# Kernel optimization log

Hardware: AMD Instinct MI355X
Metric: run time of the kernel (lower is better)

## Reference

```python
import jax, jax.numpy as jnp
import numpy as np


def silu(x):
    return x * jax.nn.sigmoid(x)


def setup_inputs() -> dict:
    key = jax.random.key(0)
    ks = jax.random.split(key, 12)
    B, S, Dm = 2, 2048, 768
    I, N, R, K = 1536, 16, 48, 4
    s = 0.02
    return {
        "input_states": jax.random.normal(ks[0], (B, S, Dm), jnp.float32),
        "in_proj_w": jax.random.normal(ks[1], (2 * I, Dm), jnp.float32) * s,
        "conv_w": jax.random.normal(ks[2], (I, 1, K), jnp.float32) * s,
        "conv_b": jax.random.normal(ks[3], (I,), jnp.float32) * s,
        "x_proj_w": jax.random.normal(ks[4], (R + 2 * N, I), jnp.float32) * s,
        "dt_proj_w": jax.random.normal(ks[5], (I, R), jnp.float32) * s,
        "dt_proj_b": jax.random.normal(ks[6], (I,), jnp.float32) * s,
        "A_log": jax.random.normal(ks[7], (I, N), jnp.float32) * 0.5,
        "D": jax.random.normal(ks[8], (I,), jnp.float32) * s,
        "out_proj_w": jax.random.normal(ks[9], (Dm, I), jnp.float32) * s,
        "alpha": jax.random.uniform(ks[10], (I,), jnp.float32),
        "feature_gating": jax.random.uniform(ks[11], (I,), jnp.float32),
    }


def reference(input_states, in_proj_w, conv_w, conv_b, x_proj_w,
              dt_proj_w, dt_proj_b, A_log, D, out_proj_w,
              alpha, feature_gating):
    Bsz, S, _ = input_states.shape
    I, N = A_log.shape
    R = dt_proj_w.shape[1]
    K = conv_w.shape[-1]

    # in_proj (no bias), chunk into hidden / gate, each [B, I, S]
    proj = jnp.einsum('bsd,ed->bse', input_states, in_proj_w)  # [B, S, 2I]
    hidden, gate = jnp.split(proj.transpose(0, 2, 1), 2, axis=1)

    # causal depthwise conv1d + SiLU
    h = jax.lax.conv_general_dilated(
        hidden, conv_w, window_strides=(1,), padding=[(K - 1, 0)],
        dimension_numbers=('NCH', 'OIH', 'NCH'), feature_group_count=I)
    h = silu(h + conv_b[None, :, None])  # [B, I, S]

    # x_proj -> time_step, B, C
    ssm_p = jnp.einsum('bis,ei->bse', h, x_proj_w)  # [B, S, R+2N]
    ts, Bm, Cm = jnp.split(ssm_p, [R, R + N], axis=-1)

    dt = jax.nn.softplus(jnp.einsum('bsr,ir->bsi', ts, dt_proj_w) + dt_proj_b)
    dt = dt.transpose(0, 2, 1)                       # [B, I, S]
    dt = dt.at[:, :, -1].multiply(alpha[None, :])    # alpha scales last step

    A = -jnp.exp(A_log.astype(jnp.float32))          # [I, N]
    dA = jnp.exp(A[None, :, None, :] * dt[:, :, :, None])       # [B, I, S, N]
    dBu = dt[:, :, :, None] * Bm[:, None, :, :] * h[:, :, :, None]  # [B, I, S, N]

    def step(state, xs):
        dA_t, dBu_t, C_t = xs
        state = dA_t * state + dBu_t                 # [B, I, N]
        y = jnp.einsum('bin,bn->bi', state, C_t)
        return state, y

    init = jnp.zeros((Bsz, I, N), input_states.dtype)
    _, ys = jax.lax.scan(
        step, init,
        (dA.transpose(2, 0, 1, 3), dBu.transpose(2, 0, 1, 3), Cm.transpose(1, 0, 2)))
    y = ys.transpose(1, 2, 0)                        # [B, I, S]

    y = (y + h * D[None, :, None]) * silu(gate)
    y = y.at[:, :, -1].multiply(feature_gating[None, :])
    return jnp.einsum('bis,di->bsd', y, out_proj_w)  # [B, S, Dm]
```

## Files before the change

kernel.cpp:

```cpp
#include <hip/hip_runtime.h>
#include <math.h>


static constexpr int S_LEN  = 2048;
static constexpr int DMODEL = 768;
static constexpr int ICH    = 1536;
static constexpr int NST    = 16;
static constexpr int MROWS  = 4096;
static constexpr int NCH    = 64;
static constexpr int CHS    = 32;
static constexpr int CSTR   = 2 * ICH * NST;

typedef _Float16 f16;
typedef f16 f16x8 __attribute__((ext_vector_type(8)));
typedef f16 f16x4 __attribute__((ext_vector_type(4)));
typedef f16 f16x2 __attribute__((ext_vector_type(2)));
typedef float f32x4 __attribute__((ext_vector_type(4)));

#if __has_builtin(__builtin_amdgcn_exp2f)
#define EXP2F(x) __builtin_amdgcn_exp2f(x)
#else
#define EXP2F(x) exp2f(x)
#endif

typedef __attribute__((address_space(3))) void lds_void;
typedef const __attribute__((address_space(1))) void glb_void;

__device__ __forceinline__ void glds16(f16* l, const f16* g) {
    __builtin_amdgcn_global_load_lds((glb_void*)g, (lds_void*)l, 16, 0, 0);
}

__device__ __forceinline__ float silu_f(float x) {
    return x / (1.0f + __expf(-x));
}

__global__ __launch_bounds__(256) void prep(
    const float* __restrict__ s0, f16* __restrict__ d0, int n0,
    const float* __restrict__ s1, f16* __restrict__ d1, int n1,
    float* __restrict__ z)
{
    int i = (blockIdx.x * 256 + threadIdx.x) * 4;
    if (i < n0) {
        float4 v = *(const float4*)(s0 + i);
        f16x4 o = { (f16)v.x, (f16)v.y, (f16)v.z, (f16)v.w };
        *(f16x4*)(d0 + i) = o;
    } else if (i < n0 + n1) {
        int j = i - n0;
        float4 v = *(const float4*)(s1 + j);
        f16x4 o = { (f16)v.x, (f16)v.y, (f16)v.z, (f16)v.w };
        *(f16x4*)(d1 + j) = o;
    } else {
        int j = i - n0 - n1;
        float4 zv = {};
        *(float4*)(z + j) = zv;
    }
}

__global__ __launch_bounds__(256) void k1m(
    const f16* __restrict__ Xh,
    const f16* __restrict__ Wh,
    f16* __restrict__ hidden,
    f16* __restrict__ sgate)
{
    __shared__ __align__(16) f16 As[2][128 * 32];
    __shared__ __align__(16) f16 Bs[2][64 * 32];
    const int tid = threadIdx.x;
    const int lane = tid & 63, wave = tid >> 6;
    const int quad = lane >> 4, l16 = lane & 15;
    const int wm = wave & 1, wn = wave >> 1;
    const int m0 = blockIdx.x * 128, n0 = blockIdx.y * 64;
    const int l_row = lane >> 2, l_c8 = (lane & 3) * 8;

    const f16* Ag = Xh + (size_t)(m0 + wave * 16 + l_row) * 768 + l_c8;
    const f16* Bg = Wh + (size_t)(n0 + wave * 16 + l_row) * 768 + l_c8;
    const int aLo = (wave * 16) * 32, aHi = (64 + wave * 16) * 32;
    const int bOff = (wave * 16) * 32;

#define K1_STAGE(buf, kk)                                        \
    do {                                                         \
        glds16(&As[buf][aLo], Ag + (kk));                        \
        glds16(&As[buf][aHi], Ag + (size_t)64 * 768 + (kk));     \
        glds16(&Bs[buf][bOff], Bg + (kk));                       \
    } while (0)

#define K1_COMPUTE(buf)                                                        \
    do {                                                                       \
        f16x8 af[4], bf[2];                                                    \
        _Pragma("unroll")                                                      \
        for (int mi = 0; mi < 4; ++mi)                                         \
            af[mi] = *(const f16x8*)&As[buf][(wm * 64 + mi * 16 + l16) * 32 + quad * 8]; \
        _Pragma("unroll")                                                      \
        for (int ni = 0; ni < 2; ++ni)                                         \
            bf[ni] = *(const f16x8*)&Bs[buf][(wn * 32 + ni * 16 + l16) * 32 + quad * 8]; \
        _Pragma("unroll")                                                      \
        for (int mi = 0; mi < 4; ++mi)                                         \
            _Pragma("unroll")                                                  \
            for (int ni = 0; ni < 2; ++ni)                                     \
                acc[mi][ni] = __builtin_amdgcn_mfma_f32_16x16x32_f16(          \
                    af[mi], bf[ni], acc[mi][ni], 0, 0, 0);                     \
    } while (0)

    K1_STAGE(0, 0);
    __syncthreads();

    f32x4 acc[4][2] = {};
    for (int k0 = 0; k0 < 768; k0 += 64) {
        K1_STAGE(1, k0 + 32);
        K1_COMPUTE(0);
        __syncthreads();
        if (k0 + 64 < 768) K1_STAGE(0, k0 + 64);
        K1_COMPUTE(1);
        __syncthreads();
    }
#undef K1_STAGE
#undef K1_COMPUTE

    const bool isGate = (n0 >= ICH);
    f16* outp = isGate ? sgate : hidden;
    const int e0 = (isGate ? (n0 - ICH) : n0) + wn * 32 + l16;
    #pragma unroll
    for (int mi = 0; mi < 4; ++mi) {
        #pragma unroll
        for (int ni = 0; ni < 2; ++ni) {
            #pragma unroll
            for (int r = 0; r < 4; ++r) {
                int m = m0 + wm * 64 + mi * 16 + quad * 4 + r;
                int e = e0 + ni * 16;
                float v = acc[mi][ni][r];
                if (isGate) v = silu_f(v);
                outp[(size_t)m * ICH + e] = (f16)v;
            }
        }
    }
}

__global__ __launch_bounds__(256) void k3m(
    const f16* __restrict__ hidden,
    const float* __restrict__ conv_w,
    const float* __restrict__ conv_b,
    const float* __restrict__ xw,
    f16* __restrict__ h,
    float* __restrict__ ssmp)
{
    __shared__ __align__(16) f16 Ah[128 * 32];
    __shared__ __align__(16) f16 Bh[80 * 32];
    __shared__ float4 cwv[96];
    __shared__ float  cbv[96];
    const int tid = threadIdx.x;
    const int lane = tid & 63, wave = tid >> 6;
    const int quad = lane >> 4, l16 = lane & 15;
    const int m0 = blockIdx.x * 128;
    const int kbeg = blockIdx.y * 96;

    if (tid < 96) {
        cwv[tid] = *(const float4*)(conv_w + (size_t)(kbeg + tid) * 4);
        cbv[tid] = conv_b[kbeg + tid];
    }

    f32x4 acc[2][5] = {};
    for (int k0 = kbeg; k0 < kbeg + 96; k0 += 32) {
        __syncthreads();
        #pragma unroll
        for (int it = 0; it < 2; ++it) {
            int slot = tid + it * 256;
            int r_ = slot >> 2, c_ = (slot & 3) * 8;
            int gm = m0 + r_, c = k0 + c_;
            int s = gm & (S_LEN - 1);
            const f16* bp = hidden + (size_t)gm * ICH + c;
            f16x8 x0 = *(const f16x8*)bp;
            f16x8 x1 = *(const f16x8*)(bp - (s >= 1 ? ICH : 0));
            f16x8 x2 = *(const f16x8*)(bp - (s >= 2 ? 2 * ICH : 0));
            f16x8 x3 = *(const f16x8*)(bp - (s >= 3 ? 3 * ICH : 0));
            f16x8 o;
            #pragma unroll
            for (int j = 0; j < 8; ++j) {
                int ci = (k0 - kbeg) + c_ + j;
                float4 w = cwv[ci];
                float v1 = (s >= 1) ? (float)x1[j] : 0.f;
                float v2 = (s >= 2) ? (float)x2[j] : 0.f;
                float v3 = (s >= 3) ? (float)x3[j] : 0.f;
                float r = cbv[ci] + w.x * v3 + w.y * v2 + w.z * v1 + w.w * (float)x0[j];
                o[j] = (f16)silu_f(r);
            }
            *(f16x8*)&Ah[r_ * 32 + c_] = o;
            *(f16x8*)(h + (size_t)gm * ICH + c) = o;
        }
        {
            int c4 = (tid & 7) * 4;
            for (int r = tid >> 3; r < 80; r += 32) {
                float4 v = *(const float4*)(xw + (size_t)r * ICH + k0 + c4);
                f16x4 o = { (f16)v.x, (f16)v.y, (f16)v.z, (f16)v.w };
                *(f16x4*)&Bh[r * 32 + c4] = o;
            }
        }
        __syncthreads();
        f16x8 af[2], bf[5];
        #pragma unroll
        for (int mi = 0; mi < 2; ++mi)
            af[mi] = *(const f16x8*)&Ah[(wave * 32 + mi * 16 + l16) * 32 + quad * 8];
        #pragma unroll
        for (int j = 0; j < 5; ++j)
            bf[j] = *(const f16x8*)&Bh[(j * 16 + l16) * 32 + quad * 8];
        #pragma unroll
        for (int mi = 0; mi < 2; ++mi)
            #pragma unroll
            for (int j = 0; j < 5; ++j)
                acc[mi][j] = __builtin_amdgcn_mfma_f32_16x16x32_f16(
                    af[mi], bf[j], acc[mi][j], 0, 0, 0);
    }
    #pragma unroll
    for (int mi = 0; mi < 2; ++mi) {
        #pragma unroll
        for (int j = 0; j < 5; ++j) {
            #pragma unroll
            for (int r = 0; r < 4; ++r) {
                int m = m0 + wave * 32 + mi * 16 + quad * 4 + r;
                atomicAdd(ssmp + (size_t)m * 80 + j * 16 + l16, acc[mi][j][r]);
            }
        }
    }
}

__global__ __launch_bounds__(256) void k4m(
    const float* __restrict__ ssmp,
    const float* __restrict__ dtw,
    const float* __restrict__ dtb,
    const float* __restrict__ alpha,
    f16* __restrict__ dt)
{
    __shared__ __align__(16) f16 As[128 * 72];
    __shared__ __align__(16) f16 Bs[128 * 72];
    const int tid = threadIdx.x;
    const int lane = tid & 63, wave = tid >> 6;
    const int quad = lane >> 4, l16 = lane & 15;
    const int wm = wave & 1, wn = wave >> 1;
    const int m0 = blockIdx.x * 128, n0 = blockIdx.y * 128;
    const int srow = tid >> 1;
    const int shalf = tid & 1;

    {
        const float* sa = ssmp + (size_t)(m0 + srow) * 80 + shalf * 24;
        const float* sb = dtw + (size_t)(n0 + srow) * 48 + shalf * 24;
        f16* da = &As[srow * 72 + shalf * 24];
        f16* db = &Bs[srow * 72 + shalf * 24];
        #pragma unroll
        for (int j = 0; j < 6; ++j) {
            float4 va = *(const float4*)(sa + 4 * j);
            float4 vb = *(const float4*)(sb + 4 * j);
            f16x4 oa = { (f16)va.x, (f16)va.y, (f16)va.z, (f16)va.w };
            f16x4 ob = { (f16)vb.x, (f16)vb.y, (f16)vb.z, (f16)vb.w };
            *(f16x4*)(da + 4 * j) = oa;
            *(f16x4*)(db + 4 * j) = ob;
        }
        if (shalf) {
            f16x8 z = {};
            *(f16x8*)&As[srow * 72 + 48] = z;
            *(f16x8*)&As[srow * 72 + 56] = z;
            *(f16x8*)&Bs[srow * 72 + 48] = z;
            *(f16x8*)&Bs[srow * 72 + 56] = z;
        }
    }
    __syncthreads();

    f32x4 acc[4][4] = {};
    #pragma unroll
    for (int ks = 0; ks < 2; ++ks) {
        f16x8 af[4], bf[4];
        #pragma unroll
        for (int mi = 0; mi < 4; ++mi)
            af[mi] = *(const f16x8*)&As[(wm * 64 + mi * 16 + l16) * 72 + ks * 32 + quad * 8];
        #pragma unroll
        for (int ni = 0; ni < 4; ++ni)
            bf[ni] = *(const f16x8*)&Bs[(wn * 64 + ni * 16 + l16) * 72 + ks * 32 + quad * 8];
        #pragma unroll
        for (int mi = 0; mi < 4; ++mi)
            #pragma unroll
            for (int ni = 0; ni < 4; ++ni)
                acc[mi][ni] = __builtin_amdgcn_mfma_f32_16x16x32_f16(
                    af[mi], bf[ni], acc[mi][ni], 0, 0, 0);
    }

    #pragma unroll
    for (int ni = 0; ni < 4; ++ni) {
        int e = n0 + wn * 64 + ni * 16 + l16;
        float bias = dtb[e];
        float al = alpha[e];
        #pragma unroll
        for (int mi = 0; mi < 4; ++mi) {
            #pragma unroll
            for (int r = 0; r < 4; ++r) {
                int m = m0 + wm * 64 + mi * 16 + quad * 4 + r;
                float x = acc[mi][ni][r] + bias;
                float sp = (x > 20.0f) ? x : __logf(1.0f + __expf(x));
                if ((m & (S_LEN - 1)) == S_LEN - 1) sp *= al;
                dt[(size_t)m * ICH + e] = (f16)sp;
            }
        }
    }
}

__global__ __launch_bounds__(256) void k5a_chunk(
    const f16* __restrict__ dt,
    const f16* __restrict__ h,
    const float* __restrict__ ssmp,
    const float* __restrict__ A_log,
    float* __restrict__ PArr,
    float* __restrict__ SfArr)
{
    __shared__ float dts[CHS * 64];
    __shared__ float hs[CHS * 64];
    __shared__ float Bc[CHS][16];
    const int tid = threadIdx.x;
    const int n4 = tid & 3;
    const int il = tid >> 2;
    const int i0 = blockIdx.x * 64;
    const int i = i0 + il;
    const int c = blockIdx.y;
    const int b = blockIdx.z;
    const int s0 = c * CHS;
    const size_t row0 = (size_t)(b * S_LEN + s0) * ICH + i0;

    {
        int r = tid >> 3, c8 = (tid & 7) * 8;
        size_t g_off = row0 + (size_t)r * ICH + c8;
        f16x8 dv = *(const f16x8*)(dt + g_off);
        f16x8 hv = *(const f16x8*)(h + g_off);
        #pragma unroll
        for (int j = 0; j < 8; ++j) {
            dts[r * 64 + c8 + j] = (float)dv[j];
            hs[r * 64 + c8 + j]  = (float)hv[j];
        }
    }
    if (tid < CHS * 4) {
        int t = tid >> 2, q = tid & 3;
        *(float4*)&Bc[t][q * 4] =
            *(const float4*)(ssmp + (size_t)(b * S_LEN + s0 + t) * 80 + 48 + q * 4);
    }

    const float L2E = 1.44269504088896f;
    float4 alv = *(const float4*)(A_log + i * NST + n4 * 4);
    float A[4] = { -__expf(alv.x) * L2E, -__expf(alv.y) * L2E,
                   -__expf(alv.z) * L2E, -__expf(alv.w) * L2E };
    float st[4] = {};
    float cdt = 0.f;
    __syncthreads();
    #pragma unroll 4
    for (int t = 0; t < CHS; ++t) {
        float dtv = dts[t * 64 + il];
        float hv  = hs[t * 64 + il];
        float4 Bv = *(const float4*)&Bc[t][n4 * 4];
        cdt += dtv;
        float x = dtv * hv;
        #pragma unroll
        for (int j = 0; j < 4; ++j) {
            float dA = EXP2F(A[j] * dtv);
            st[j] = fmaf(dA, st[j], x * (&Bv.x)[j]);
        }
    }
    size_t base = (size_t)c * CSTR + (size_t)(b * ICH + i) * NST + n4 * 4;
    float4 Pv = { EXP2F(A[0] * cdt), EXP2F(A[1] * cdt),
                  EXP2F(A[2] * cdt), EXP2F(A[3] * cdt) };
    float4 Sv = { st[0], st[1], st[2], st[3] };
    *(float4*)(PArr + base)  = Pv;
    *(float4*)(SfArr + base) = Sv;
}

__global__ __launch_bounds__(256) void k5b_carry(
    const float* PArr,
    const float* __restrict__ SfArr,
    float* CIn)
{
    int idx = blockIdx.x * 256 + threadIdx.x;
    float p[NCH], s[NCH];
    #pragma unroll
    for (int c = 0; c < NCH; ++c) {
        size_t a = (size_t)c * CSTR + idx;
        p[c] = PArr[a];
        s[c] = SfArr[a];
    }
    float carry = 0.f;
    #pragma unroll
    for (int c = 0; c < NCH; ++c) {
        CIn[(size_t)c * CSTR + idx] = carry;
        carry = fmaf(p[c], carry, s[c]);
    }
}

__global__ __launch_bounds__(256) void k5c_emit(
    const f16* __restrict__ dt,
    const f16* __restrict__ h,
    const f16* __restrict__ sgate,
    const float* __restrict__ ssmp,
    const float* __restrict__ A_log,
    const float* __restrict__ Dp,
    const float* __restrict__ fg,
    const float* __restrict__ CIn,
    f16* __restrict__ yh)
{
    __shared__ float dts[CHS * 64];
    __shared__ float hs[CHS * 64];
    __shared__ float gs[CHS * 64];
    __shared__ float BC[CHS][32];
    const int tid = threadIdx.x;
    const int n4 = tid & 3;
    const int il = tid >> 2;
    const int i0 = blockIdx.x * 64;
    const int i = i0 + il;
    const int c = blockIdx.y;
    const int b = blockIdx.z;
    const int s0 = c * CHS;
    const size_t row0 = (size_t)(b * S_LEN + s0) * ICH + i0;

    {
        int r = tid >> 3, c8 = (tid & 7) * 8;
        size_t g_off = row0 + (size_t)r * ICH + c8;
        f16x8 dv = *(const f16x8*)(dt + g_off);
        f16x8 hv = *(const f16x8*)(h + g_off);
        f16x8 gv = *(const f16x8*)(sgate + g_off);
        #pragma unroll
        for (int j = 0; j < 8; ++j) {
            dts[r * 64 + c8 + j] = (float)dv[j];
            hs[r * 64 + c8 + j]  = (float)hv[j];
            gs[r * 64 + c8 + j]  = (float)gv[j];
        }
    }
    {
        int t = tid >> 3, q = tid & 7;
        *(float4*)&BC[t][q * 4] =
            *(const float4*)(ssmp + (size_t)(b * S_LEN + s0 + t) * 80 + 48 + q * 4);
    }

    const float L2E = 1.44269504088896f;
    float4 alv = *(const float4*)(A_log + i * NST + n4 * 4);
    float A[4] = { -__expf(alv.x) * L2E, -__expf(alv.y) * L2E,
                   -__expf(alv.z) * L2E, -__expf(alv.w) * L2E };
    const float Dv = Dp[i];
    const float fgv = fg[i];
    float4 civ = *(const float4*)(CIn + (size_t)c * CSTR + (size_t)(b * ICH + i) * NST + n4 * 4);
    float st[4] = { civ.x, civ.y, civ.z, civ.w };
    f16* yout = yh + row0 + il;
    const bool last_chunk = (c == NCH - 1);
    __syncthreads();
    #pragma unroll 4
    for (int t = 0; t < CHS; ++t) {
        float dtv = dts[t * 64 + il];
        float hv  = hs[t * 64 + il];
        float4 Bv = *(const float4*)&BC[t][n4 * 4];
        float4 Cv = *(const float4*)&BC[t][16 + n4 * 4];
        float x = dtv * hv;
        float yp = 0.f;
        #pragma unroll
        for (int j = 0; j < 4; ++j) {
            float dA = EXP2F(A[j] * dtv);
            st[j] = fmaf(dA, st[j], x * (&Bv.x)[j]);
            yp = fmaf(st[j], (&Cv.x)[j], yp);
        }
        yp += __shfl_xor(yp, 1, 4);
        yp += __shfl_xor(yp, 2, 4);
        if (n4 == 0) {
            float yv = fmaf(hv, Dv, yp) * gs[t * 64 + il];
            if (last_chunk && t == CHS - 1) yv *= fgv;
            yout[(size_t)t * ICH] = (f16)yv;
        }
    }
}

__global__ __launch_bounds__(256) void k6m(
    const f16* __restrict__ Yh,
    const float* __restrict__ OWf,
    float* __restrict__ out)
{
    __shared__ __align__(16) f16 As[2][64 * 32];
    __shared__ __align__(16) f16 Bs[2][64 * 32];
    const int tid = threadIdx.x;
    const int lane = tid & 63, wave = tid >> 6;
    const int quad = lane >> 4, l16 = lane & 15;
    const int wm = wave & 1, wn = wave >> 1;
    const int m0 = blockIdx.x * 64, n0 = blockIdx.y * 64;
    const int l_row = lane >> 2, l_c8 = (lane & 3) * 8;

    const f16* Ag = Yh + (size_t)(m0 + wave * 16 + l_row) * ICH + l_c8;
    const int aOff = (wave * 16) * 32;
    const int brow = tid >> 2, bc8 = (tid & 3) * 8;
    const float* Bgf = OWf + (size_t)(n0 + brow) * ICH + bc8;
    float4 vb0, vb1;

#define K6_STAGEA(buf, kk) glds16(&As[buf][aOff], Ag + (kk))

#define K6_LOADB(kk)                                             \
    do {                                                         \
        vb0 = *(const float4*)(Bgf + (kk));                      \
        vb1 = *(const float4*)(Bgf + (kk) + 4);                  \
    } while (0)

#define K6_WRITEB(buf)                                                         \
    do {                                                                       \
        f16x8 o = { (f16)vb0.x, (f16)vb0.y, (f16)vb0.z, (f16)vb0.w,            \
                    (f16)vb1.x, (f16)vb1.y, (f16)vb1.z, (f16)vb1.w };          \
        *(f16x8*)&Bs[buf][brow * 32 + bc8] = o;                                \
    } while (0)

#define K6_COMPUTE(buf)                                                        \
    do {                                                                       \
        f16x8 af[2], bf[2];                                                    \
        _Pragma("unroll")                                                      \
        for (int mi = 0; mi < 2; ++mi)                                         \
            af[mi] = *(const f16x8*)&As[buf][(wm * 32 + mi * 16 + l16) * 32 + quad * 8]; \
        _Pragma("unroll")                                                      \
        for (int ni = 0; ni < 2; ++ni)                                         \
            bf[ni] = *(const f16x8*)&Bs[buf][(wn * 32 + ni * 16 + l16) * 32 + quad * 8]; \
        _Pragma("unroll")                                                      \
        for (int mi = 0; mi < 2; ++mi)                                         \
            _Pragma("unroll")                                                  \
            for (int ni = 0; ni < 2; ++ni)                                     \
                acc[mi][ni] = __builtin_amdgcn_mfma_f32_16x16x32_f16(          \
                    af[mi], bf[ni], acc[mi][ni], 0, 0, 0);                     \
    } while (0)

    K6_STAGEA(0, 0);
    K6_LOADB(0);
    K6_WRITEB(0);
    __syncthreads();

    f32x4 acc[2][2] = {};
    for (int k0 = 0; k0 < ICH; k0 += 64) {
        K6_STAGEA(1, k0 + 32);
        K6_LOADB(k0 + 32);
        K6_COMPUTE(0);
        K6_WRITEB(1);
        __syncthreads();
        if (k0 + 64 < ICH) {
            K6_STAGEA(0, k0 + 64);
            K6_LOADB(k0 + 64);
        }
        K6_COMPUTE(1);
        if (k0 + 64 < ICH) K6_WRITEB(0);
        __syncthreads();
    }
#undef K6_STAGEA
#undef K6_LOADB
#undef K6_WRITEB
#undef K6_COMPUTE

    #pragma unroll
    for (int mi = 0; mi < 2; ++mi) {
        #pragma unroll
        for (int ni = 0; ni < 2; ++ni) {
            #pragma unroll
            for (int r = 0; r < 4; ++r) {
                int m = m0 + wm * 32 + mi * 16 + quad * 4 + r;
                int d = n0 + wn * 32 + ni * 16 + l16;
                out[(size_t)m * DMODEL + d] = acc[mi][ni][r];
            }
        }
    }
}

extern "C" void kernel_launch(void* const* d_in, const int* in_sizes, int n_in,
                              void* d_out, int out_size, void* d_ws, size_t ws_size,
                              hipStream_t stream) {
    const float* X     = (const float*)d_in[0];
    const float* W1    = (const float*)d_in[1];
    const float* CW    = (const float*)d_in[2];
    const float* CB    = (const float*)d_in[3];
    const float* XW    = (const float*)d_in[4];
    const float* DTW   = (const float*)d_in[5];
    const float* DTB   = (const float*)d_in[6];
    const float* ALOG  = (const float*)d_in[7];
    const float* DD    = (const float*)d_in[8];
    const float* OW    = (const float*)d_in[9];
    const float* ALPHA = (const float*)d_in[10];
    const float* FG    = (const float*)d_in[11];
    float* out = (float*)d_out;

    const size_t NBI = (size_t)MROWS * ICH;
    f16* hidden_h = (f16*)d_ws;
    f16* sgate_h  = hidden_h + NBI;
    f16* h_h      = sgate_h + NBI;
    f16* dt_h     = h_h + NBI;
    float* ssmp   = (float*)(dt_h + NBI);
    f16* Xh       = (f16*)(ssmp + (size_t)MROWS * 80);
    f16* W1h      = Xh + (size_t)MROWS * DMODEL;
    float* SfA    = (float*)(W1h + (size_t)2 * ICH * DMODEL);
    float* PArr = (float*)hidden_h;
    float* CIn  = PArr;
    f16* yh     = (f16*)SfA;

    const int nX = MROWS * DMODEL;
    const int nW1 = 2 * ICH * DMODEL;
    const int nS = MROWS * 80;
    prep<<<dim3((nX + nW1 + nS) / 1024), 256, 0, stream>>>(X, Xh, nX, W1, W1h, nW1, ssmp);
    k1m<<<dim3(32, 48), 256, 0, stream>>>(Xh, W1h, hidden_h, sgate_h);
    k3m<<<dim3(32, 16), 256, 0, stream>>>(hidden_h, CW, CB, XW, h_h, ssmp);
    k4m<<<dim3(32, 12), 256, 0, stream>>>(ssmp, DTW, DTB, ALPHA, dt_h);
    k5a_chunk<<<dim3(24, NCH, 2), 256, 0, stream>>>(dt_h, h_h, ssmp, ALOG, PArr, SfA);
    k5b_carry<<<dim3(192), 256, 0, stream>>>(PArr, SfA, CIn);
    k5c_emit<<<dim3(24, NCH, 2), 256, 0, stream>>>(dt_h, h_h, sgate_h, ssmp, ALOG, DD, FG, CIn, yh);
    k6m<<<dim3(64, 12), 256, 0, stream>>>(yh, OW, out);
}
```

Before: 245.6 us.

## Restructure out_proj GEMM to process two K-slabs per barrier with padded B tile

The out_proj GEMM kernel now keeps four shared-memory slabs and processes two 32-wide K slices between each barrier, halving the number of __syncthreads calls. Global loads for the next pair are issued before computing the current pair. The B tile row stride is padded from 32 to 40 halves to reduce LDS bank conflicts on the MFMA fragment reads. This uses more LDS and registers per block, which could lower occupancy.

```diff
diff --git a/kernel.cpp b/kernel.cpp
--- a/kernel.cpp
+++ b/kernel.cpp
@@ -470,8 +470,8 @@
     const float* __restrict__ OWf,
     float* __restrict__ out)
 {
-    __shared__ __align__(16) f16 As[2][64 * 32];
-    __shared__ __align__(16) f16 Bs[2][64 * 32];
+    __shared__ __align__(16) f16 As[4][64 * 32];
+    __shared__ __align__(16) f16 Bs[4][64 * 40];
     const int tid = threadIdx.x;
     const int lane = tid & 63, wave = tid >> 6;
     const int quad = lane >> 4, l16 = lane & 15;
@@ -483,32 +483,37 @@
     const int aOff = (wave * 16) * 32;
     const int brow = tid >> 2, bc8 = (tid & 3) * 8;
     const float* Bgf = OWf + (size_t)(n0 + brow) * ICH + bc8;
-    float4 vb0, vb1;
-
-#define K6_STAGEA(buf, kk) glds16(&As[buf][aOff], Ag + (kk))
-
-#define K6_LOADB(kk)                                             \
+    float4 vb0, vb1, vb2, vb3;
+
+#define K6_STAGEA(hb, kk) glds16(&As[hb][aOff], Ag + (kk))
+
+#define K6_LOADB2(kk)                                            \
     do {                                                         \
         vb0 = *(const float4*)(Bgf + (kk));                      \
         vb1 = *(const float4*)(Bgf + (kk) + 4);                  \
+        vb2 = *(const float4*)(Bgf + (kk) + 32);                 \
+        vb3 = *(const float4*)(Bgf + (kk) + 36);                 \
     } while (0)
 
-#define K6_WRITEB(buf)                                                         \
+#define K6_WRITEB2(hb0, hb1)                                                   \
     do {                                                                       \
-        f16x8 o = { (f16)vb0.x, (f16)vb0.y, (f16)vb0.z, (f16)vb0.w,            \
-                    (f16)vb1.x, (f16)vb1.y, (f16)vb1.z, (f16)vb1.w };          \
-        *(f16x8*)&Bs[buf][brow * 32 + bc8] = o;                                \
+        f16x8 o0 = { (f16)vb0.x, (f16)vb0.y, (f16)vb0.z, (f16)vb0.w,           \
+                     (f16)vb1.x, (f16)vb1.y, (f16)vb1.z, (f16)vb1.w };         \
+        f16x8 o1 = { (f16)vb2.x, (f16)vb2.y, (f16)vb2.z, (f16)vb2.w,           \
+                     (f16)vb3.x, (f16)vb3.y, (f16)vb3.z, (f16)vb3.w };         \
+        *(f16x8*)&Bs[hb0][brow * 40 + bc8] = o0;                               \
+        *(f16x8*)&Bs[hb1][brow * 40 + bc8] = o1;                               \
     } while (0)
 
-#define K6_COMPUTE(buf)                                                        \
+#define K6_COMPUTE(hb)                                                         \
     do {                                                                       \
         f16x8 af[2], bf[2];                                                    \
         _Pragma("unroll")                                                      \
         for (int mi = 0; mi < 2; ++mi)                                         \
-            af[mi] = *(const f16x8*)&As[buf][(wm * 32 + mi * 16 + l16) * 32 + quad * 8]; \
+            af[mi] = *(const f16x8*)&As[hb][(wm * 32 + mi * 16 + l16) * 32 + quad * 8]; \
         _Pragma("unroll")                                                      \
         for (int ni = 0; ni < 2; ++ni)                                         \
-            bf[ni] = *(const f16x8*)&Bs[buf][(wn * 32 + ni * 16 + l16) * 32 + quad * 8]; \
+            bf[ni] = *(const f16x8*)&Bs[hb][(wn * 32 + ni * 16 + l16) * 40 + quad * 8]; \
         _Pragma("unroll")                                                      \
         for (int mi = 0; mi < 2; ++mi)                                         \
             _Pragma("unroll")                                                  \
@@ -518,28 +523,27 @@
     } while (0)
 
     K6_STAGEA(0, 0);
-    K6_LOADB(0);
-    K6_WRITEB(0);
+    K6_STAGEA(1, 32);
+    K6_LOADB2(0);
+    K6_WRITEB2(0, 1);
     __syncthreads();
 
     f32x4 acc[2][2] = {};
-    for (int k0 = 0; k0 < ICH; k0 += 64) {
-        K6_STAGEA(1, k0 + 32);
-        K6_LOADB(k0 + 32);
-        K6_COMPUTE(0);
-        K6_WRITEB(1);
+    for (int h = 0; h < 48; h += 2) {
+        const bool more = (h + 2 < 48);
+        if (more) {
+            K6_STAGEA((h + 2) & 3, (h + 2) * 32);
+            K6_STAGEA((h + 3) & 3, (h + 3) * 32);
+            K6_LOADB2((h + 2) * 32);
+        }
+        K6_COMPUTE(h & 3);
+        K6_COMPUTE((h + 1) & 3);
+        if (more) K6_WRITEB2((h + 2) & 3, (h + 3) & 3);
         __syncthreads();
-        if (k0 + 64 < ICH) {
-            K6_STAGEA(0, k0 + 64);
-            K6_LOADB(k0 + 64);
-        }
-        K6_COMPUTE(1);
-        if (k0 + 64 < ICH) K6_WRITEB(0);
-        __syncthreads();
     }
 #undef K6_STAGEA
-#undef K6_LOADB
-#undef K6_WRITEB
+#undef K6_LOADB2
+#undef K6_WRITEB2
 #undef K6_COMPUTE
 
     #pragma unroll
```

After: 241.5 us. No clear change (-1.7%).
